# Kernel optimization log

Hardware: AMD Instinct MI355X
Metric: run time of the kernel (lower is better)

## Reference

```python
import jax, jax.numpy as jnp
import numpy as np

B, T, D = 8, 4096, 64

def setup_inputs() -> dict:
    key = jax.random.key(0)
    k1, k2 = jax.random.split(key)
    inputs = jax.random.normal(k1, (B, T, D), dtype=jnp.float32)
    # keras 'random_normal' initializer: stddev 0.05
    W = jax.random.normal(k2, (D, D), dtype=jnp.float32) * 0.05
    return {"inputs": inputs, "W": W}

def reference(inputs, W):
    # q = inputs @ W               : [B,T,D]
    # a = q @ inputs^T             : [B,T,T] (no scaling, bias b unused in original)
    # out = softmax(a, -1) @ inputs: [B,T,D]
    q = jnp.einsum('btd,de->bte', inputs, W)
    scores = jnp.einsum('btd,bsd->bts', q, inputs)
    attn = jax.nn.softmax(scores, axis=-1)
    return jnp.einsum('bts,bsd->btd', attn, inputs)
```

## Files before the change

kernel.cpp:

```cpp
#include <hip/hip_runtime.h>

typedef _Float16 f16;
typedef _Float16 f16x8 __attribute__((ext_vector_type(8)));
typedef __bf16 bf16x8 __attribute__((ext_vector_type(8)));
typedef float floatx4 __attribute__((ext_vector_type(4)));
typedef unsigned short u16;

#define B_N   8
#define T_SEQ 4096
#define DIM   64
#define QT    64
#define NIT2  32
#define XSTR  72
#define LOG2E 1.44269504f
#define FRAG  512

#if __has_builtin(__builtin_amdgcn_exp2f)
#define EXP2(x) __builtin_amdgcn_exp2f(x)
#else
#define EXP2(x) exp2f(x)
#endif

__launch_bounds__(256, 2)
__global__ void prep_kernel(const float* __restrict__ X, const float* __restrict__ W,
                            u16* __restrict__ Kswz, u16* __restrict__ Qswz,
                            u16* __restrict__ Vswz) {
  __shared__ __attribute__((aligned(16))) u16 Xs[DIM * XSTR];
  __shared__ __attribute__((aligned(16))) u16 Wt[DIM * XSTR];
  __shared__ __attribute__((aligned(16))) u16 Qs[DIM * XSTR];
  const int tid = threadIdx.x;
  const int lane = tid & 63, w = tid >> 6, qd = lane >> 4, ln = lane & 15;
  const int b = blockIdx.y;
  const int t0 = blockIdx.x * 64;
  const long xbase = ((long)b * T_SEQ + t0) * DIM;

  {
    const int r = tid >> 2, c0 = (tid & 3) * 16;
    float v[16];
#pragma unroll
    for (int i = 0; i < 4; i++)
      *(float4*)&v[i * 4] = *(const float4*)(X + xbase + (long)r * DIM + c0 + i * 4);
    u16 h[16];
#pragma unroll
    for (int j = 0; j < 16; j++) h[j] = __builtin_bit_cast(u16, (f16)v[j]);
    *(uint4*)&Xs[r * XSTR + c0] = *(uint4*)&h[0];
    *(uint4*)&Xs[r * XSTR + c0 + 8] = *(uint4*)&h[8];
    float wv[16];
#pragma unroll
    for (int i = 0; i < 4; i++)
      *(float4*)&wv[i * 4] = *(const float4*)(W + r * DIM + c0 + i * 4);
#pragma unroll
    for (int j = 0; j < 16; j++) Wt[(c0 + j) * XSTR + r] = __builtin_bit_cast(u16, (f16)wv[j]);
  }
  __syncthreads();

  {
    const int tile = w >> 1, ct = w & 1;
    const int krow = tile * 32 + (ln >> 2) * 8 + ct * 4 + (ln & 3);
    const long F = ((long)b * 128 + blockIdx.x * 2 + tile) * 2 + ct;
#pragma unroll
    for (int ks = 0; ks < 2; ks++) {
      f16x8 kv = *(const f16x8*)&Xs[krow * XSTR + ks * 32 + qd * 8];
      *(f16x8*)(Kswz + (F * 2 + ks) * FRAG + lane * 8) = kv;
    }
  }

  {
    const int wq = w * 16;
    floatx4 acc[4];
#pragma unroll
    for (int ct = 0; ct < 4; ct++) acc[ct] = (floatx4)0.0f;
#pragma unroll
    for (int ks = 0; ks < 2; ks++) {
      f16x8 aX = *(const f16x8*)&Xs[(wq + ln) * XSTR + ks * 32 + qd * 8];
#pragma unroll
      for (int ct = 0; ct < 4; ct++) {
        f16x8 bW = *(const f16x8*)&Wt[(ct * 16 + ln) * XSTR + ks * 32 + qd * 8];
        acc[ct] = __builtin_amdgcn_mfma_f32_16x16x32_f16(aX, bW, acc[ct], 0, 0, 0);
      }
    }
#pragma unroll
    for (int ct = 0; ct < 4; ct++)
#pragma unroll
      for (int r = 0; r < 4; r++)
        Qs[(wq + qd * 4 + r) * XSTR + ct * 16 + ln] =
            __builtin_bit_cast(u16, (f16)(acc[ct][r] * LOG2E));
  }

  {
    const long Cb = (long)b * 4 + w;
    const int J0 = blockIdx.x * 2;
#pragma unroll
    for (int J = 0; J < 2; J++) {
      bf16x8 vv;
#pragma unroll
      for (int j = 0; j < 8; j++) {
        f16 hv = __builtin_bit_cast(f16, Xs[(J * 32 + qd * 8 + j) * XSTR + w * 16 + ln]);
        vv[j] = (__bf16)(float)hv;
      }
      *(bf16x8*)(Vswz + (Cb * (T_SEQ / 32) + J0 + J) * FRAG + lane * 8) = vv;
    }
  }

  {
    const long R = (long)b * (T_SEQ / 16) + blockIdx.x * 4 + w;
#pragma unroll
    for (int ks = 0; ks < 2; ks++) {
      f16x8 qv = *(const f16x8*)&Qs[(w * 16 + ln) * XSTR + ks * 32 + qd * 8];
      *(f16x8*)(Qswz + (R * 2 + ks) * FRAG + lane * 8) = qv;
    }
  }
}

__launch_bounds__(512, 4)
__global__ void attn_kernel(const u16* __restrict__ Kswz, const u16* __restrict__ Qswz,
                            const u16* __restrict__ Vswz, float* __restrict__ out) {
  __shared__ __attribute__((aligned(16))) float Opart[8][16][68];
  __shared__ float lpart[8][32];

  const int tid = threadIdx.x;
  const int lane = tid & 63;
  const int w = tid >> 6;
  const int qd = lane >> 4;
  const int ln = lane & 15;
  const int wg = w >> 2;
  const int wk = w & 3;
  const int bid = blockIdx.x;
  const int b = bid & 7;
  const int q0 = (bid >> 3) * QT;
  const long bbase = (long)b * T_SEQ * DIM;

  f16x8 aQ[2][2];
#pragma unroll
  for (int rb = 0; rb < 2; rb++)
#pragma unroll
    for (int ks = 0; ks < 2; ks++)
      aQ[rb][ks] = *(const f16x8*)(Qswz +
          (((long)b * (T_SEQ / 16) + (q0 >> 4) + wg * 2 + rb) * 2 + ks) * FRAG + lane * 8);

  const u16* pK = Kswz + ((long)b * 128 + wk) * 4 * FRAG + lane * 8;
  const u16* pV = Vswz + ((long)b * 4 * 128 + wk) * FRAG + lane * 8;

  floatx4 O[2][4];
  float lacc[2] = {0.f, 0.f};
#pragma unroll
  for (int rb = 0; rb < 2; rb++)
#pragma unroll
    for (int db = 0; db < 4; db++) O[rb][db] = (floatx4)0.0f;

#pragma unroll 1
  for (int kt = 0; kt < NIT2; kt++) {
    f16x8 bK[2][2];
#pragma unroll
    for (int ct = 0; ct < 2; ct++)
#pragma unroll
      for (int ks = 0; ks < 2; ks++)
        bK[ct][ks] = *(const f16x8*)(pK + ((long)kt * 16 + ct * 2 + ks) * FRAG);

    bf16x8 bV[4];
#pragma unroll
    for (int db = 0; db < 4; db++)
      bV[db] = *(const bf16x8*)(pV + ((long)kt * 4 + (long)db * 128) * FRAG);

    floatx4 St[2][2];
#pragma unroll
    for (int ct = 0; ct < 2; ct++)
#pragma unroll
      for (int rb = 0; rb < 2; rb++) St[ct][rb] = (floatx4)0.0f;
#pragma unroll
    for (int ks = 0; ks < 2; ks++)
#pragma unroll
      for (int ct = 0; ct < 2; ct++)
#pragma unroll
        for (int rb = 0; rb < 2; rb++)
          St[ct][rb] = __builtin_amdgcn_mfma_f32_16x16x32_f16(bK[ct][ks], aQ[rb][ks], St[ct][rb], 0, 0, 0);

    bf16x8 pk[2];
#pragma unroll
    for (int rb = 0; rb < 2; rb++) {
      float ps = 0.f;
#pragma unroll
      for (int ct = 0; ct < 2; ct++)
#pragma unroll
        for (int r = 0; r < 4; r++) {
          float p = EXP2(St[ct][rb][r]);
          ps += p;
          pk[rb][ct * 4 + r] = (__bf16)p;
        }
      lacc[rb] += ps;
    }

#pragma unroll
    for (int rb = 0; rb < 2; rb++)
#pragma unroll
      for (int db = 0; db < 4; db++)
        O[rb][db] = __builtin_amdgcn_mfma_f32_16x16x32_bf16(pk[rb], bV[db], O[rb][db], 0, 0, 0);
  }

#pragma unroll
  for (int rb = 0; rb < 2; rb++) {
    float v = lacc[rb];
    v += __shfl_xor(v, 16, 64);
    v += __shfl_xor(v, 32, 64);
    if (qd == 0) lpart[w][rb * 16 + ln] = v;
  }

#pragma unroll 1
  for (int rb = 0; rb < 2; rb++) {
    __syncthreads();
#pragma unroll
    for (int db = 0; db < 4; db++)
#pragma unroll
      for (int r = 0; r < 4; r++)
        Opart[w][qd * 4 + r][db * 16 + ln] = O[rb][db][r];
    __syncthreads();
    const int wg2 = tid >> 8;
    const int q2 = (tid >> 4) & 15;
    const int d0 = (tid & 15) * 4;
    float4 s = *(const float4*)&Opart[wg2 * 4 + 0][q2][d0];
    const float4 s1 = *(const float4*)&Opart[wg2 * 4 + 1][q2][d0];
    const float4 s2 = *(const float4*)&Opart[wg2 * 4 + 2][q2][d0];
    const float4 s3 = *(const float4*)&Opart[wg2 * 4 + 3][q2][d0];
    float l = lpart[wg2 * 4 + 0][rb * 16 + q2] + lpart[wg2 * 4 + 1][rb * 16 + q2] +
              lpart[wg2 * 4 + 2][rb * 16 + q2] + lpart[wg2 * 4 + 3][rb * 16 + q2];
    const float inv = 1.0f / l;
    float4 o;
    o.x = (s.x + s1.x + s2.x + s3.x) * inv;
    o.y = (s.y + s1.y + s2.y + s3.y) * inv;
    o.z = (s.z + s1.z + s2.z + s3.z) * inv;
    o.w = (s.w + s1.w + s2.w + s3.w) * inv;
    *(float4*)(out + bbase + (long)(q0 + wg2 * 32 + rb * 16 + q2) * DIM + d0) = o;
  }
}

extern "C" void kernel_launch(void* const* d_in, const int* in_sizes, int n_in,
                              void* d_out, int out_size, void* d_ws, size_t ws_size,
                              hipStream_t stream) {
  const float* X = (const float*)d_in[0];
  const float* W = (const float*)d_in[1];
  float* out = (float*)d_out;
  const size_t SZ = (size_t)B_N * T_SEQ * DIM * 2;
  u16* Kswz = (u16*)d_ws;
  u16* Qswz = (u16*)((char*)d_ws + SZ);
  u16* Vswz = (u16*)((char*)d_ws + 2 * SZ);
  prep_kernel<<<dim3(T_SEQ / 64, B_N), 256, 0, stream>>>(X, W, Kswz, Qswz, Vswz);
  attn_kernel<<<dim3(B_N * (T_SEQ / QT)), 512, 0, stream>>>(Kswz, Qswz, Vswz, out);
}
```

Baseline: 116.7 us.

## Double-buffer K/V tiles in LDS via async global_load_lds in attention loop

Replaces the per-wave direct global loads of swizzled K and V fragments with cooperative asynchronous global-to-LDS copies into a double-buffered 64 KB shared buffer. Waves 0-3 stage K and waves 4-7 stage V for the next tile while the current tile is computed. Each wave group previously loaded the same K/V data separately, so this also removes duplicate global traffic. It wraps the MFMA blocks in s_setprio to favour matrix issue. The cost is a block-wide barrier every iteration and much larger LDS use, which may reduce occupancy below the four-block launch bound.

```diff
diff --git a/kernel.cpp b/kernel.cpp
--- a/kernel.cpp
+++ b/kernel.cpp
@@ -10,7 +10,7 @@
 #define T_SEQ 4096
 #define DIM   64
 #define QT    64
-#define NIT2  32
+#define NIT   32
 #define XSTR  72
 #define LOG2E 1.44269504f
 #define FRAG  512
@@ -20,6 +20,9 @@
 #else
 #define EXP2(x) exp2f(x)
 #endif
+
+typedef __attribute__((address_space(1))) const void gvoid;
+typedef __attribute__((address_space(3))) void svoid;
 
 __launch_bounds__(256, 2)
 __global__ void prep_kernel(const float* __restrict__ X, const float* __restrict__ W,
@@ -115,8 +118,9 @@
 __launch_bounds__(512, 4)
 __global__ void attn_kernel(const u16* __restrict__ Kswz, const u16* __restrict__ Qswz,
                             const u16* __restrict__ Vswz, float* __restrict__ out) {
-  __shared__ __attribute__((aligned(16))) float Opart[8][16][68];
+  __shared__ __attribute__((aligned(16))) char sbuf[2][32768];
   __shared__ float lpart[8][32];
+  float* Opart = (float*)&sbuf[0][0];
 
   const int tid = threadIdx.x;
   const int lane = tid & 63;
@@ -138,8 +142,25 @@
       aQ[rb][ks] = *(const f16x8*)(Qswz +
           (((long)b * (T_SEQ / 16) + (q0 >> 4) + wg * 2 + rb) * 2 + ks) * FRAG + lane * 8);
 
-  const u16* pK = Kswz + ((long)b * 128 + wk) * 4 * FRAG + lane * 8;
-  const u16* pV = Vswz + ((long)b * 4 * 128 + wk) * FRAG + lane * 8;
+  const char* gKw = (const char*)Kswz + (long)b * 524288 + (long)w * 4096 + lane * 16;
+  const char* gVw = (const char*)Vswz + (long)b * 524288 + (long)(w - 4) * 1024 + lane * 16;
+
+#define STAGE(bufv, t)                                                                  \
+  do {                                                                                  \
+    if (w < 4) {                                                                        \
+      const char* g = gKw + (long)(t) * 16384;                                          \
+      char* l = &sbuf[bufv][w * 4096];                                                  \
+      _Pragma("unroll") for (int i = 0; i < 4; i++)                                     \
+          __builtin_amdgcn_global_load_lds((gvoid*)(g + i * 1024), (svoid*)(l + i * 1024), \
+                                           16, 0, 0);                                   \
+    } else {                                                                            \
+      const char* g = gVw + (long)(t) * 4096;                                           \
+      char* l = &sbuf[bufv][16384 + (w - 4) * 4096];                                    \
+      _Pragma("unroll") for (int i = 0; i < 4; i++)                                     \
+          __builtin_amdgcn_global_load_lds((gvoid*)(g + i * 131072), (svoid*)(l + i * 1024), \
+                                           16, 0, 0);                                   \
+    }                                                                                   \
+  } while (0)
 
   floatx4 O[2][4];
   float lacc[2] = {0.f, 0.f};
@@ -148,25 +169,33 @@
 #pragma unroll
     for (int db = 0; db < 4; db++) O[rb][db] = (floatx4)0.0f;
 
+  STAGE(0, 0);
+  __syncthreads();
+
+  int buf = 0;
 #pragma unroll 1
-  for (int kt = 0; kt < NIT2; kt++) {
+  for (int t = 0; t < NIT; t++) {
+    if (t + 1 < NIT) STAGE(buf ^ 1, t + 1);
+
+    const char* Kb = &sbuf[buf][wk * 4096];
+    const char* Vb = &sbuf[buf][16384 + wk * 4096];
     f16x8 bK[2][2];
 #pragma unroll
     for (int ct = 0; ct < 2; ct++)
 #pragma unroll
       for (int ks = 0; ks < 2; ks++)
-        bK[ct][ks] = *(const f16x8*)(pK + ((long)kt * 16 + ct * 2 + ks) * FRAG);
-
+        bK[ct][ks] = *(const f16x8*)(Kb + (ct * 2 + ks) * 1024 + lane * 16);
     bf16x8 bV[4];
 #pragma unroll
     for (int db = 0; db < 4; db++)
-      bV[db] = *(const bf16x8*)(pV + ((long)kt * 4 + (long)db * 128) * FRAG);
+      bV[db] = *(const bf16x8*)(Vb + db * 1024 + lane * 16);
 
     floatx4 St[2][2];
 #pragma unroll
     for (int ct = 0; ct < 2; ct++)
 #pragma unroll
       for (int rb = 0; rb < 2; rb++) St[ct][rb] = (floatx4)0.0f;
+    __builtin_amdgcn_s_setprio(1);
 #pragma unroll
     for (int ks = 0; ks < 2; ks++)
 #pragma unroll
@@ -174,6 +203,7 @@
 #pragma unroll
         for (int rb = 0; rb < 2; rb++)
           St[ct][rb] = __builtin_amdgcn_mfma_f32_16x16x32_f16(bK[ct][ks], aQ[rb][ks], St[ct][rb], 0, 0, 0);
+    __builtin_amdgcn_s_setprio(0);
 
     bf16x8 pk[2];
 #pragma unroll
@@ -190,11 +220,16 @@
       lacc[rb] += ps;
     }
 
+    __builtin_amdgcn_s_setprio(1);
 #pragma unroll
     for (int rb = 0; rb < 2; rb++)
 #pragma unroll
       for (int db = 0; db < 4; db++)
         O[rb][db] = __builtin_amdgcn_mfma_f32_16x16x32_bf16(pk[rb], bV[db], O[rb][db], 0, 0, 0);
+    __builtin_amdgcn_s_setprio(0);
+
+    __syncthreads();
+    buf ^= 1;
   }
 
 #pragma unroll
@@ -212,15 +247,15 @@
     for (int db = 0; db < 4; db++)
 #pragma unroll
       for (int r = 0; r < 4; r++)
-        Opart[w][qd * 4 + r][db * 16 + ln] = O[rb][db][r];
+        Opart[(w * 16 + qd * 4 + r) * 68 + db * 16 + ln] = O[rb][db][r];
     __syncthreads();
     const int wg2 = tid >> 8;
     const int q2 = (tid >> 4) & 15;
     const int d0 = (tid & 15) * 4;
-    float4 s = *(const float4*)&Opart[wg2 * 4 + 0][q2][d0];
-    const float4 s1 = *(const float4*)&Opart[wg2 * 4 + 1][q2][d0];
-    const float4 s2 = *(const float4*)&Opart[wg2 * 4 + 2][q2][d0];
-    const float4 s3 = *(const float4*)&Opart[wg2 * 4 + 3][q2][d0];
+    float4 s = *(const float4*)&Opart[((wg2 * 4 + 0) * 16 + q2) * 68 + d0];
+    const float4 s1 = *(const float4*)&Opart[((wg2 * 4 + 1) * 16 + q2) * 68 + d0];
+    const float4 s2 = *(const float4*)&Opart[((wg2 * 4 + 2) * 16 + q2) * 68 + d0];
+    const float4 s3 = *(const float4*)&Opart[((wg2 * 4 + 3) * 16 + q2) * 68 + d0];
     float l = lpart[wg2 * 4 + 0][rb * 16 + q2] + lpart[wg2 * 4 + 1][rb * 16 + q2] +
               lpart[wg2 * 4 + 2][rb * 16 + q2] + lpart[wg2 * 4 + 3][rb * 16 + q2];
     const float inv = 1.0f / l;
@@ -231,6 +266,7 @@
     o.w = (s.w + s1.w + s2.w + s3.w) * inv;
     *(float4*)(out + bbase + (long)(q0 + wg2 * 32 + rb * 16 + q2) * DIM + d0) = o;
   }
+#undef STAGE
 }
 
 extern "C" void kernel_launch(void* const* d_in, const int* in_sizes, int n_in,
```

Result: slower. 221.7 us (+89.9%).
